# Kernel optimization log

Hardware: AMD Instinct MI355X
Metric: run time of the kernel (lower is better)

## Reference

```python
import jax, jax.numpy as jnp
import numpy as np

# ---- static config (matches init_kwargs) ----
B, N, DIM = 1, 2048, 1024
H, KVH, D = 16, 8, 64
GQ = H // KVH                 # grouped queries per kv head
WS = 64                       # sliding window size (causal, exact)
CBS, STRIDE = 32, 16          # compress block size / sliding stride
SEL_BLK, NSEL, NMEM = 32, 4, 1
NCB = N // STRIDE             # num compressed blocks (128)
NFB = N // SEL_BLK            # num fine blocks (64)
NCPF = SEL_BLK // STRIDE      # compressed blocks per fine block (2)
HID = CBS * D                 # compress MLP hidden (expand factor 1.0)
SCALE = D ** -0.5
THETA = 10000.0
NEG = -jnp.finfo(jnp.float32).max


def setup_inputs():
    key = jax.random.key(0)
    ks = jax.random.split(key, 16)
    s = 0.02
    r = lambda i, shape: jax.random.normal(ks[i], shape, jnp.float32) * s
    return {
        "inp": jax.random.normal(ks[0], (B, N, DIM), jnp.float32),
        "norm_g": jnp.ones((DIM,), jnp.float32),
        "Wqkv": r(1, (DIM, (H + 2 * KVH) * D)),
        "mem_kv": r(2, (2, KVH, NMEM, D)),
        "k_pos": r(3, (KVH, CBS, D)),
        "v_pos": r(4, (KVH, CBS, D)),
        "kW1": r(5, (CBS * D, HID)), "kb1": jnp.zeros((HID,), jnp.float32),
        "kW2": r(6, (HID, D)), "kb2": jnp.zeros((D,), jnp.float32),
        "vW1": r(7, (CBS * D, HID)), "vb1": jnp.zeros((HID,), jnp.float32),
        "vW2": r(8, (HID, D)), "vb2": jnp.zeros((D,), jnp.float32),
        "combW": r(9, (DIM, 3 * H)),
        "combB": jnp.tile(jnp.array([-2.0, -2.0, 2.0], jnp.float32), H),
        "Wout": r(10, (H * D, DIM)),
    }


def _rope(t):
    # lucidrains rotary-embedding-torch: interleaved adjacent-pair rotation
    inv_freq = 1.0 / (THETA ** (jnp.arange(0, D, 2, dtype=jnp.float32) / D))
    ang = jnp.arange(N, dtype=jnp.float32)[:, None] * inv_freq        # [N, D/2]
    cos = jnp.repeat(jnp.cos(ang), 2, axis=-1)                        # [N, D]
    sin = jnp.repeat(jnp.sin(ang), 2, axis=-1)
    t2 = t.reshape(*t.shape[:-1], D // 2, 2)
    rot = jnp.stack([-t2[..., 1], t2[..., 0]], axis=-1).reshape(t.shape)
    return t * cos + rot * sin


def _forward(inp, norm_g, Wqkv, mem_kv, k_pos, v_pos,
             kW1, kb1, kW2, kb2, vW1, vb1, vW2, vb2,
             combW, combB, Wout):
    # RMSNorm
    x = inp * jax.lax.rsqrt(jnp.mean(inp * inp, -1, keepdims=True)
                            + jnp.finfo(inp.dtype).eps) * norm_g
    qkv = x @ Wqkv
    q, k, v = jnp.split(qkv, [H * D, H * D + KVH * D], axis=-1)
    q = q.reshape(B, N, H, D).transpose(0, 2, 1, 3)      # b h n d
    k = k.reshape(B, N, KVH, D).transpose(0, 2, 1, 3)    # b kvh n d
    v = v.reshape(B, N, KVH, D).transpose(0, 2, 1, 3)

    # ---- compressed branch (overlapping windows, left zero pad) ----
    overlap = CBS - STRIDE
    kp = jnp.pad(k, ((0, 0), (0, 0), (overlap, 0), (0, 0)))
    vp = jnp.pad(v, ((0, 0), (0, 0), (overlap, 0), (0, 0)))
    widx = jnp.arange(NCB)[:, None] * STRIDE + jnp.arange(CBS)[None, :]  # [NCB, CBS]
    kw = kp[:, :, widx] + k_pos[None, :, None]   # b kvh w cbs d
    vw = vp[:, :, widx] + v_pos[None, :, None]

    def cmlp(t, W1, b1, W2, b2):
        t = t.reshape(B, KVH, NCB, CBS * D)
        return jax.nn.relu(t @ W1 + b1) @ W2 + b2       # b kvh w d

    ck = cmlp(kw, kW1, kb1, kW2, kb2)
    cv = cmlp(vw, vW1, vb1, vW2, vb2)
    ck = jnp.concatenate([jnp.broadcast_to(mem_kv[0], (B, KVH, NMEM, D)), ck], 2)
    cv = jnp.concatenate([jnp.broadcast_to(mem_kv[1], (B, KVH, NMEM, D)), cv], 2)

    qg = q.reshape(B, KVH, GQ, N, D)
    csim = jnp.einsum('bhgid,bhjd->bhgij', qg, ck) * SCALE   # no mask (cmask=None)
    cattn = jax.nn.softmax(csim, -1)
    cout = jnp.einsum('bhgij,bhjd->bhgid', cattn, cv).reshape(B, H, N, D)

    # rotary AFTER compressed attention (as in source)
    rq, rk = _rope(q), _rope(k)

    # ---- importance scores -> top-k fine block selection ----
    imp = csim[..., NMEM:].mean(2)                          # b kvh n NCB (share grouped q)
    imp = imp.reshape(B, KVH, N, NFB, NCPF).mean(-1)        # mean-pool to fine blocks
    q_blk = jnp.arange(N) // SEL_BLK
    diag = q_blk[:, None] == jnp.arange(NFB)[None, :]
    imp = jnp.where(diag[None, None], NEG, imp)             # mask own (diagonal) block
    imp = jax.nn.softmax(jnp.pad(imp, ((0, 0),) * 3 + ((1, 0),),
                                 constant_values=-1000.0), -1)[..., 1:]
    sel_val, sel_idx = jax.lax.top_k(imp, NSEL)             # b kvh n NSEL

    # ---- fine (block-selected) attention ----
    own = jnp.broadcast_to(q_blk[None, None, :, None], (B, KVH, N, 1))
    sel_idx = jnp.concatenate([sel_idx, own], -1)           # append own block
    fmask = jnp.repeat((sel_val > 1e-10)[..., None], SEL_BLK, -1)  # b kvh n NSEL blk
    causal_row = jnp.tril(jnp.ones((SEL_BLK, SEL_BLK), bool))[jnp.arange(N) % SEL_BLK]
    causal = jnp.broadcast_to(causal_row[None, None, :, None, :],
                              (B, KVH, N, 1, SEL_BLK))
    fmask = jnp.concatenate([fmask, causal], 3).reshape(B, KVH, N, (NSEL + 1) * SEL_BLK)

    fk_blocks = rk.reshape(B, KVH, NFB, SEL_BLK, D)
    fv_blocks = v.reshape(B, KVH, NFB, SEL_BLK, D)
    gather = jax.vmap(jax.vmap(lambda blocks, idx: blocks[idx]))  # over b, kvh
    fk = gather(fk_blocks, sel_idx).reshape(B, KVH, N, (NSEL + 1) * SEL_BLK, D)
    fv = gather(fv_blocks, sel_idx).reshape(B, KVH, N, (NSEL + 1) * SEL_BLK, D)

    rqg = rq.reshape(B, KVH, GQ, N, D)
    fsim = jnp.einsum('bhgid,bhijd->bhgij', rqg, fk) * SCALE
    fsim = jnp.where(fmask[:, :, None], fsim, NEG / 10)
    fattn = jax.nn.softmax(fsim, -1)
    fout = jnp.einsum('bhgij,bhijd->bhgid', fattn, fv).reshape(B, H, N, D)

    # ---- sliding window (causal, exact window size WS) ----
    NW = N // WS
    kp2 = jnp.pad(rk, ((0, 0), (0, 0), (WS, 0), (0, 0)))
    vp2 = jnp.pad(v, ((0, 0), (0, 0), (WS, 0), (0, 0)))
    kidx = jnp.arange(NW)[:, None] * WS + jnp.arange(2 * WS)[None, :]
    kwin = kp2[:, :, kidx]                                  # b kvh nw 2ws d
    vwin = vp2[:, :, kidx]
    qwin = rqg.reshape(B, KVH, GQ, NW, WS, D)
    ssim = jnp.einsum('bhgwid,bhwjd->bhgwij', qwin, kwin) * SCALE
    i = jnp.arange(WS)[:, None]
    j = jnp.arange(2 * WS)[None, :]
    diff = i - (j - WS)
    local_ok = (diff >= 0) & (diff < WS)                    # [WS, 2WS]
    keypos = jnp.arange(NW)[:, None, None] * WS + (jnp.arange(2 * WS) - WS)[None, None, :]
    smask = local_ok[None] & (keypos >= 0)                  # [NW, WS, 2WS]
    ssim = jnp.where(smask[None, None, None], ssim, NEG)
    sattn = jax.nn.softmax(ssim, -1)
    sout = jnp.einsum('bhgwij,bhwjd->bhgwid', sattn, vwin).reshape(B, H, N, D)

    # ---- learned strategy combination (compressed, fine, sliding) ----
    gates = jax.nn.sigmoid(x @ combW + combB).reshape(B, N, H, 3).transpose(0, 2, 1, 3)
    out = gates[..., 0:1] * cout + gates[..., 1:2] * fout + gates[..., 2:3] * sout
    out = out.transpose(0, 2, 1, 3).reshape(B, N, H * D) @ Wout
    return out


def reference(inp, norm_g, Wqkv, mem_kv, k_pos, v_pos,
              kW1, kb1, kW2, kb2, vW1, vb1, vW2, vb2,
              combW, combB, Wout):
    return _forward(inp, norm_g, Wqkv, mem_kv, k_pos, v_pos,
                    kW1, kb1, kW2, kb2, vW1, vb1, vW2, vb2,
                    combW, combB, Wout)
```

## Files before the change

### kernel.cpp

```cpp
#include <hip/hip_runtime.h>
#include <hip/hip_bf16.h>

#define NTOK 2048
#define DIM 1024
#define NH 16
#define KVH 8
#define GQ 2
#define HD 64
#define WS 64
#define CBS 32
#define STRIDE 16
#define SEL_BLK 32
#define NSEL 4
#define NMEM 1
#define NCB 128
#define NFB 64
#define HIDN 2048
#define SCALE 0.125f
#define NEGF (-3.4028234663852886e38f)
#define NEG10F (-3.4028234663852886e37f)

typedef __attribute__((ext_vector_type(8))) short bf16x8;
typedef __attribute__((ext_vector_type(4))) float f32x4;

__device__ __forceinline__ float bflo(unsigned u) { return __uint_as_float(u << 16); }
__device__ __forceinline__ float bfhi(unsigned u) { return __uint_as_float(u & 0xffff0000u); }
__device__ __forceinline__ void dot8(const float4& qa, const float4& qb, uint4 a, float& s) {
    s += qa.x * bflo(a.x) + qa.y * bfhi(a.x) + qa.z * bflo(a.y) + qa.w * bfhi(a.y) +
         qb.x * bflo(a.z) + qb.y * bfhi(a.z) + qb.z * bflo(a.w) + qb.w * bfhi(a.w);
}

__device__ __forceinline__ void gload_lds16(const void* g, void* l) {
    __builtin_amdgcn_global_load_lds((const __attribute__((address_space(1))) unsigned*)g,
                                     (__attribute__((address_space(3))) unsigned*)l, 16, 0, 0);
}

__device__ __forceinline__ void rms_body(const float* __restrict__ inp,
                                         const float* __restrict__ g,
                                         float* __restrict__ x,
                                         __hip_bfloat16* __restrict__ xb, int n) {
    const float* row = inp + (size_t)n * DIM;
    float ss = 0.f;
    for (int c = threadIdx.x; c < DIM; c += 256) { float v = row[c]; ss += v * v; }
    __shared__ float red[4];
    for (int o = 32; o; o >>= 1) ss += __shfl_down(ss, o, 64);
    if ((threadIdx.x & 63) == 0) red[threadIdx.x >> 6] = ss;
    __syncthreads();
    if (threadIdx.x == 0) red[0] = red[0] + red[1] + red[2] + red[3];
    __syncthreads();
    float rs = 1.0f / sqrtf(red[0] / (float)DIM + 1.1920928955078125e-07f);
    float* xr = x + (size_t)n * DIM;
    __hip_bfloat16* xbr = xb + (size_t)n * DIM;
    for (int c = threadIdx.x; c < DIM; c += 256) {
        float v = row[c] * rs * g[c];
        xr[c] = v;
        xbr[c] = __float2bfloat16(v);
    }
}

__device__ __forceinline__ void transpose_body(const float* __restrict__ B,
                                               __hip_bfloat16* __restrict__ Bt,
                                               int K, int N, int bx, int by) {
    __shared__ float tile[32][33];
    int n0 = bx * 32, k0 = by * 32;
    int x = threadIdx.x & 31, y = threadIdx.x >> 5;
    for (int i = 0; i < 4; i++) {
        int k = k0 + y + 8 * i, n = n0 + x;
        tile[y + 8 * i][x] = (k < K && n < N) ? B[(size_t)k * N + n] : 0.f;
    }
    __syncthreads();
    for (int i = 0; i < 4; i++) {
        int n = n0 + y + 8 * i, k = k0 + x;
        if (n < N && k < K) Bt[(size_t)n * K + k] = __float2bfloat16(tile[x][y + 8 * i]);
    }
}

__global__ __launch_bounds__(256) void pre_kernel(
    const float* inp, const float* norm_g, float* x, __hip_bfloat16* xb,
    const float* Wqkv, __hip_bfloat16* Wqkvt,
    const float* kW1, __hip_bfloat16* kW1t,
    const float* vW1, __hip_bfloat16* vW1t,
    const float* Wout, __hip_bfloat16* Woutt,
    const float* combW, __hip_bfloat16* combWt,
    const float* kW2, __hip_bfloat16* kW2t,
    const float* vW2, __hip_bfloat16* vW2t,
    const float* combB, float* gatesb,
    const float* kb2, float* ckraw,
    const float* vb2, float* cvraw) {
    int b = blockIdx.x;
    if (b < 2048) { rms_body(inp, norm_g, x, xb, b); return; }
    b -= 2048;
    if (b < 2048) { transpose_body(Wqkv, Wqkvt, 1024, 2048, b % 64, b / 64); return; }
    b -= 2048;
    if (b < 4096) { transpose_body(kW1, kW1t, 2048, 2048, b % 64, b / 64); return; }
    b -= 4096;
    if (b < 4096) { transpose_body(vW1, vW1t, 2048, 2048, b % 64, b / 64); return; }
    b -= 4096;
    if (b < 1024) { transpose_body(Wout, Woutt, 1024, 1024, b % 32, b / 32); return; }
    b -= 1024;
    if (b < 64) { transpose_body(combW, combWt, 1024, 48, b % 2, b / 2); return; }
    b -= 64;
    if (b < 128) { transpose_body(kW2, kW2t, 2048, 64, b % 2, b / 2); return; }
    b -= 128;
    if (b < 128) { transpose_body(vW2, vW2t, 2048, 64, b % 2, b / 2); return; }
    b -= 128;
    if (b < 384) {
        int idx = b * 256 + threadIdx.x;
        if (idx < 2048 * 48) gatesb[idx] = combB[idx % 48];
        return;
    }
    b -= 384;
    {
        int idx = b * 256 + threadIdx.x;
        int tot = 1024 * 64;
        if (idx < tot) ckraw[idx] = kb2[idx % 64];
        else if (idx < 2 * tot) { idx -= tot; cvraw[idx] = vb2[idx % 64]; }
        return;
    }
}
#define PRE_BLOCKS (2048 + 2048 + 4096 + 4096 + 1024 + 64 + 128 + 128 + 384 + 512)

template <int ACT, int OUTBF16>
__device__ __forceinline__ void mfma_gemm_body(const __hip_bfloat16* __restrict__ A,
                                               const __hip_bfloat16* __restrict__ Bt,
                                               const float* __restrict__ bias,
                                               void* __restrict__ Cp,
                                               int M, int N, int K, int bx, int by) {
    __shared__ __align__(16) short As[128 * 32];
    __shared__ __align__(16) short Bs[128 * 32];
    int tid = threadIdx.x;
    int lane = tid & 63, wave = tid >> 6;
    int wm = (wave >> 1) * 64, wn = (wave & 1) * 64;
    int m0 = by * 128, n0 = bx * 128;
    f32x4 acc[4][4];
    for (int r = 0; r < 4; r++)
        for (int c = 0; c < 4; c++)
            acc[r][c] = (f32x4){0.f, 0.f, 0.f, 0.f};

    int r0 = tid >> 2, kc0 = (tid & 3) * 8;
    int r1 = r0 + 64;

    for (int k0 = 0; k0 < K; k0 += 32) {
        __syncthreads();
        gload_lds16(A + (size_t)(m0 + r0) * K + k0 + kc0, &As[r0 * 32 + kc0]);
        gload_lds16(A + (size_t)(m0 + r1) * K + k0 + kc0, &As[r1 * 32 + kc0]);
        gload_lds16(Bt + (size_t)(n0 + r0) * K + k0 + kc0, &Bs[r0 * 32 + kc0]);
        gload_lds16(Bt + (size_t)(n0 + r1) * K + k0 + kc0, &Bs[r1 * 32 + kc0]);
        __syncthreads();
        bf16x8 af[4], bfr[4];
#pragma unroll
        for (int r = 0; r < 4; r++)
            af[r] = *(const bf16x8*)&As[(wm + r * 16 + (lane & 15)) * 32 + (lane >> 4) * 8];
#pragma unroll
        for (int c = 0; c < 4; c++)
            bfr[c] = *(const bf16x8*)&Bs[(wn + c * 16 + (lane & 15)) * 32 + (lane >> 4) * 8];
#pragma unroll
        for (int r = 0; r < 4; r++)
#pragma unroll
            for (int c = 0; c < 4; c++)
                acc[r][c] = __builtin_amdgcn_mfma_f32_16x16x32_bf16(af[r], bfr[c], acc[r][c], 0, 0, 0);
    }
    for (int r = 0; r < 4; r++) {
        int grow = m0 + wm + r * 16 + (lane >> 4) * 4;
        for (int c = 0; c < 4; c++) {
            int gcol = n0 + wn + c * 16 + (lane & 15);
            float bv = bias ? bias[gcol] : 0.f;
#pragma unroll
            for (int v = 0; v < 4; v++) {
                float val = acc[r][c][v] + bv;
                if (ACT == 1) val = fmaxf(val, 0.f);
                if (OUTBF16)
                    ((__hip_bfloat16*)Cp)[(size_t)(grow + v) * N + gcol] = __float2bfloat16(val);
                else
                    ((float*)Cp)[(size_t)(grow + v) * N + gcol] = val;
            }
        }
    }
}

template <int ACT, int OUTBF16>
__global__ __launch_bounds__(256) void mfma_gemm(const __hip_bfloat16* __restrict__ A,
                                                 const __hip_bfloat16* __restrict__ Bt,
                                                 const float* __restrict__ bias,
                                                 void* __restrict__ Cp,
                                                 int M, int N, int K) {
    mfma_gemm_body<ACT, OUTBF16>(A, Bt, bias, Cp, M, N, K, blockIdx.x, blockIdx.y);
}

__global__ __launch_bounds__(256) void mfma_gemm_pair(const __hip_bfloat16* A0,
                                                      const __hip_bfloat16* A1,
                                                      const __hip_bfloat16* Bt0,
                                                      const __hip_bfloat16* Bt1,
                                                      const float* bias0, const float* bias1,
                                                      __hip_bfloat16* C0, __hip_bfloat16* C1,
                                                      int M, int N, int K) {
    if (blockIdx.z == 0)
        mfma_gemm_body<1, 1>(A0, Bt0, bias0, C0, M, N, K, blockIdx.x, blockIdx.y);
    else
        mfma_gemm_body<1, 1>(A1, Bt1, bias1, C1, M, N, K, blockIdx.x, blockIdx.y);
}

__device__ __forceinline__ void skgemm_body(const __hip_bfloat16* __restrict__ A,
                                            const __hip_bfloat16* __restrict__ Bt,
                                            float* __restrict__ C,
                                            int M, int Nout, int K, int by, int bz, int nz) {
    __shared__ __align__(16) short As2[128 * 32];
    __shared__ __align__(16) short Bs2[64 * 32];
    int tid = threadIdx.x;
    int lane = tid & 63, wave = tid >> 6;
    int m0 = by * 128;
    int wm = wave * 32;
    int kchunk = K / nz;
    int kbase = bz * kchunk;
    f32x4 acc[2][4];
    for (int r = 0; r < 2; r++)
        for (int c = 0; c < 4; c++) acc[r][c] = (f32x4){0.f, 0.f, 0.f, 0.f};

    int ra = tid >> 2, kc = (tid & 3) * 8;
    int rb = ra < Nout ? ra : Nout - 1;
    for (int k0 = kbase; k0 < kbase + kchunk; k0 += 32) {
        __syncthreads();
        gload_lds16(A + (size_t)(m0 + ra) * K + k0 + kc, &As2[ra * 32 + kc]);
        gload_lds16(A + (size_t)(m0 + ra + 64) * K + k0 + kc, &As2[(ra + 64) * 32 + kc]);
        gload_lds16(Bt + (size_t)rb * K + k0 + kc, &Bs2[ra * 32 + kc]);
        __syncthreads();
        bf16x8 af[2], bfr[4];
#pragma unroll
        for (int r = 0; r < 2; r++)
            af[r] = *(const bf16x8*)&As2[(wm + r * 16 + (lane & 15)) * 32 + (lane >> 4) * 8];
#pragma unroll
        for (int c = 0; c < 4; c++)
            bfr[c] = *(const bf16x8*)&Bs2[(c * 16 + (lane & 15)) * 32 + (lane >> 4) * 8];
#pragma unroll
        for (int r = 0; r < 2; r++)
#pragma unroll
            for (int c = 0; c < 4; c++)
                acc[r][c] = __builtin_amdgcn_mfma_f32_16x16x32_bf16(af[r], bfr[c], acc[r][c], 0, 0, 0);
    }
    for (int r = 0; r < 2; r++) {
        int grow = m0 + wm + r * 16 + (lane >> 4) * 4;
        for (int c = 0; c < 4; c++) {
            int gcol = c * 16 + (lane & 15);
            if (gcol >= Nout) continue;
#pragma unroll
            for (int v = 0; v < 4; v++)
                atomicAdd(&C[(size_t)(grow + v) * Nout + gcol], acc[r][c][v]);
        }
    }
}

__global__ __launch_bounds__(256) void qkv_gates_kernel(const __hip_bfloat16* xb,
                                                        const __hip_bfloat16* Wqkvt,
                                                        float* qkv,
                                                        const __hip_bfloat16* combWt,
                                                        float* gatesb) {
    int b = blockIdx.x;
    if (b < 256) {
        mfma_gemm_body<0, 0>(xb, Wqkvt, nullptr, qkv, 2048, 2048, 1024, b & 15, b >> 4);
    } else {
        int s = b - 256;
        skgemm_body(xb, combWt, gatesb, 2048, 48, 1024, s & 15, s >> 4, 4);
    }
}

__global__ __launch_bounds__(256) void skgemm_pair(const __hip_bfloat16* A0,
                                                   const __hip_bfloat16* A1,
                                                   const __hip_bfloat16* Bt0,
                                                   const __hip_bfloat16* Bt1,
                                                   float* C0, float* C1,
                                                   int M, int Nout, int K) {
    if (blockIdx.x == 0)
        skgemm_body(A0, Bt0, C0, M, Nout, K, blockIdx.y, blockIdx.z, gridDim.z);
    else
        skgemm_body(A1, Bt1, C1, M, Nout, K, blockIdx.y, blockIdx.z, gridDim.z);
}

__global__ __launch_bounds__(256) void winrope_kernel(const float* __restrict__ qkv,
                                                      const float* __restrict__ k_pos,
                                                      const float* __restrict__ v_pos,
                                                      __hip_bfloat16* __restrict__ kwflat,
                                                      __hip_bfloat16* __restrict__ vwflat,
                                                      float* __restrict__ rq,
                                                      __hip_bfloat16* __restrict__ rk,
                                                      __hip_bfloat16* __restrict__ vt) {
    int b = blockIdx.x;
    int t = threadIdx.x;
    if (b < 4096) {
        size_t total = (size_t)(KVH * NCB) * HIDN;
        for (size_t e = (size_t)b * 256 + t; e < total; e += (size_t)4096 * 256) {
            int r = (int)(e >> 11);
            int c = (int)(e & 2047);
            int j = c >> 6, d = c & 63;
            int h = r >> 7, i = r & 127;
            int p = i * STRIDE + j - (CBS - STRIDE);
            float kb = k_pos[((size_t)h * CBS + j) * HD + d];
            float vb = v_pos[((size_t)h * CBS + j) * HD + d];
            float kv = 0.f, vv = 0.f;
            if (p >= 0) {
                kv = qkv[(size_t)p * 2048 + 1024 + h * HD + d];
                vv = qkv[(size_t)p * 2048 + 1536 + h * HD + d];
            }
            kwflat[e] = __float2bfloat16(kv + kb);
            vwflat[e] = __float2bfloat16(vv + vb);
        }
        return;
    }
    int n = b - 4096;
    for (int idx = t; idx < NH * 32; idx += 256) {
        int h = idx >> 5, f = idx & 31;
        float inv = exp2f((float)f * -0.41524101186092f);
        float ang = (float)n * inv;
        float cc = cosf(ang), ssn = sinf(ang);
        float a = qkv[(size_t)n * 2048 + h * HD + 2 * f];
        float bq = qkv[(size_t)n * 2048 + h * HD + 2 * f + 1];
        float* o = rq + ((size_t)h * NTOK + n) * HD + 2 * f;
        o[0] = a * cc - bq * ssn;
        o[1] = bq * cc + a * ssn;
    }
    for (int idx = t; idx < KVH * 32; idx += 256) {
        int h = idx >> 5, f = idx & 31;
        float inv = exp2f((float)f * -0.41524101186092f);
        float ang = (float)n * inv;
        float cc = cosf(ang), ssn = sinf(ang);
        float a = qkv[(size_t)n * 2048 + 1024 + h * HD + 2 * f];
        float bq = qkv[(size_t)n * 2048 + 1024 + h * HD + 2 * f + 1];
        __hip_bfloat16* o = rk + ((size_t)h * NTOK + n) * HD + 2 * f;
        o[0] = __float2bfloat16(a * cc - bq * ssn);
        o[1] = __float2bfloat16(bq * cc + a * ssn);
    }
    for (int idx = t; idx < KVH * HD; idx += 256) {
        int h = idx >> 6, d = idx & 63;
        vt[((size_t)h * NTOK + n) * HD + d] =
            __float2bfloat16(qkv[(size_t)n * 2048 + 1536 + h * HD + d]);
    }
}

__global__ __launch_bounds__(256) void cattn2_kernel(const float* __restrict__ qkv,
                                                     const float* __restrict__ ckraw,
                                                     const float* __restrict__ cvraw,
                                                     const float* __restrict__ memkv,
                                                     float* __restrict__ cout,
                                                     int* __restrict__ selidx,
                                                     int* __restrict__ selmask) {
    int h = blockIdx.x >> 6;
    int i0 = (blockIdx.x & 63) * 32;
    int t = threadIdx.x;
    __shared__ float qs[64][68];
    __shared__ float sc[64][132];
    __shared__ float scratch[32 * 68];
    __shared__ float memk[64], memv[64];

    for (int idx = t; idx < 4096; idx += 256) {
        int row = idx >> 6, d = idx & 63;
        int g = row >> 5, qi = row & 31;
        qs[row][d] = qkv[(size_t)(i0 + qi) * 2048 + (h * 2 + g) * 64 + d];
    }
    if (t < 64) { memk[t] = memkv[h * 64 + t]; memv[t] = memkv[(8 + h) * 64 + t]; }
    __syncthreads();
    if (t < 64) {
        float s = 0.f;
        for (int d = 0; d < 64; d++) s += qs[t][d] * memk[d];
        sc[t][0] = s * SCALE;
    }
    int rg = t >> 3, kg = t & 7;
    for (int c = 0; c < 4; c++) {
        __syncthreads();
        for (int idx = t; idx < 2048; idx += 256) {
            int jj = idx >> 6, d = idx & 63;
            scratch[jj * 68 + d] = ckraw[((size_t)h * 128 + c * 32 + jj) * 64 + d];
        }
        __syncthreads();
        float a0[4] = {}, a1[4] = {};
        for (int d = 0; d < 64; d += 4) {
            float4 q0 = *(const float4*)&qs[rg * 2][d];
            float4 q1 = *(const float4*)&qs[rg * 2 + 1][d];
#pragma unroll
            for (int kk = 0; kk < 4; kk++) {
                float4 kv = *(const float4*)&scratch[(kg + kk * 8) * 68 + d];
                a0[kk] += q0.x * kv.x + q0.y * kv.y + q0.z * kv.z + q0.w * kv.w;
                a1[kk] += q1.x * kv.x + q1.y * kv.y + q1.z * kv.z + q1.w * kv.w;
            }
        }
#pragma unroll
        for (int kk = 0; kk < 4; kk++) {
            sc[rg * 2][1 + c * 32 + kg + kk * 8] = a0[kk] * SCALE;
            sc[rg * 2 + 1][1 + c * 32 + kg + kk * 8] = a1[kk] * SCALE;
        }
    }
    __syncthreads();
    for (int idx = t; idx < 2048; idx += 256) {
        int qi = idx >> 6, fb = idx & 63;
        float v = 0.25f * (sc[qi][1 + 2 * fb] + sc[qi][2 + 2 * fb] +
                           sc[32 + qi][1 + 2 * fb] + sc[32 + qi][2 + 2 * fb]);
        if (fb == ((i0 + qi) >> 5)) v = NEGF;
        scratch[qi * 66 + fb] = v;
    }
    __syncthreads();
    if (t < 32) {
        float* row = &scratch[t * 66];
        float m = -1000.f;
        for (int j = 0; j < 64; j++) m = fmaxf(m, row[j]);
        float den = __expf(-1000.f - m);
        for (int j = 0; j < 64; j++) den += __expf(row[j] - m);
        float invd = 1.f / den;
        unsigned long long taken = 0ull;
        int mk = 0;
        size_t base = ((size_t)h * NTOK + i0 + t) * 5;
        for (int p = 0; p < NSEL; p++) {
            float bv = NEGF;
            int bi = 0;
            for (int j = 0; j < 64; j++) {
                if (!((taken >> j) & 1ull) && row[j] > bv) { bv = row[j]; bi = j; }
            }
            taken |= 1ull << bi;
            selidx[base + p] = bi;
            if (__expf(bv - m) * invd > 1e-10f) mk |= 1 << p;
        }
        selidx[base + 4] = (i0 + t) >> 5;
        selmask[h * NTOK + i0 + t] = mk;
    } else if (t >= 64 && t < 128) {
        int r = t - 64;
        float m = NEGF;
        for (int j = 0; j < 129; j++) m = fmaxf(m, sc[r][j]);
        float den = 0.f;
        for (int j = 0; j < 129; j++) { float e = __expf(sc[r][j] - m); sc[r][j] = e; den += e; }
        float inv = 1.f / den;
        for (int j = 0; j < 129; j++) sc[r][j] *= inv;
    }
    __syncthreads();
    int dg = t & 7;
    float o0[8], o1[8];
    {
        float p0 = sc[rg * 2][0], p1 = sc[rg * 2 + 1][0];
#pragma unroll
        for (int dd = 0; dd < 8; dd++) {
            float v = memv[dg + dd * 8];
            o0[dd] = p0 * v;
            o1[dd] = p1 * v;
        }
    }
    for (int c = 0; c < 4; c++) {
        __syncthreads();
        for (int idx = t; idx < 2048; idx += 256) {
            int jj = idx >> 6, d = idx & 63;
            scratch[jj * 68 + d] = cvraw[((size_t)h * 128 + c * 32 + jj) * 64 + d];
        }
        __syncthreads();
        for (int jj = 0; jj < 32; jj++) {
            float p0 = sc[rg * 2][1 + c * 32 + jj];
            float p1 = sc[rg * 2 + 1][1 + c * 32 + jj];
#pragma unroll
            for (int dd = 0; dd < 8; dd++) {
                float v = scratch[jj * 68 + dg + dd * 8];
                o0[dd] += p0 * v;
                o1[dd] += p1 * v;
            }
        }
    }
    {
        int row = rg * 2;
        int g = row >> 5, qi = row & 31;
        int g2 = (row + 1) >> 5, qi2 = (row + 1) & 31;
#pragma unroll
        for (int dd = 0; dd < 8; dd++) {
            cout[(((size_t)(h * 2 + g)) * NTOK + i0 + qi) * 64 + dd * 8 + dg] = o0[dd];
            cout[(((size_t)(h * 2 + g2)) * NTOK + i0 + qi2) * 64 + dd * 8 + dg] = o1[dd];
        }
    }
}

#define SWROWPAD 72
__global__ __launch_bounds__(256) void attn_fused2_kernel(const float* __restrict__ rq,
                                                          const __hip_bfloat16* __restrict__ rk,
                                                          const __hip_bfloat16* __restrict__ vt,
                                                          const int* __restrict__ selidx,
                                                          const int* __restrict__ selmask,
                                                          float* __restrict__ fout,
                                                          float* __restrict__ sout) {
    int tid = threadIdx.x;
    int ws = tid >> 6, lane = tid & 63;
    __shared__ __align__(16) char smem[2 * 128 * SWROWPAD * 2 + 4 * 128 * 4];
    __shared__ int sel[4][5];
    __shared__ int smk[4];

    int kq = lane >> 2, c = lane & 3;
    int kv8 = lane >> 3, c8 = lane & 7;

    if (blockIdx.x < 256) {
        int h = blockIdx.x >> 5;
        int q0 = (blockIdx.x & 31) * 64;
        short* ks = (short*)smem;
        short* vs = ks + 128 * SWROWPAD;
        float* ps = (float*)(vs + 128 * SWROWPAD);
        int basek = q0 - 63;
        for (int idx = tid; idx < 127 * 8; idx += 256) {
            int row = idx >> 3, ch = (idx & 7) * 8;
            int kpos = basek + row;
            uint4 kv = (uint4){0u, 0u, 0u, 0u}, vv = (uint4){0u, 0u, 0u, 0u};
            if (kpos >= 0) {
                kv = *(const uint4*)(rk + ((size_t)h * NTOK + kpos) * 64 + ch);
                vv = *(const uint4*)(vt + ((size_t)h * NTOK + kpos) * 64 + ch);
            }
            *(uint4*)&ks[row * SWROWPAD + ch] = kv;
            *(uint4*)&vs[row * SWROWPAD + ch] = vv;
        }
        __syncthreads();
        float* p0 = ps + ws * 128;
        float* p1 = p0 + 64;
#pragma unroll 1
        for (int tq = 0; tq < 16; tq++) {
            int i = q0 + ws * 16 + tq;
            int ibase = ws * 16 + tq;
            const float* q0p = rq + ((size_t)(h * 2 + 0) * NTOK + i) * 64 + c * 16;
            const float* q1p = rq + ((size_t)(h * 2 + 1) * NTOK + i) * 64 + c * 16;
            float4 qa[4], qb[4];
#pragma unroll
            for (int u = 0; u < 4; u++) {
                qa[u] = *(const float4*)(q0p + u * 4);
                qb[u] = *(const float4*)(q1p + u * 4);
            }
#pragma unroll
            for (int kt = 0; kt < 4; kt++) {
                int key = kt * 16 + kq;
                const short* kr = &ks[(ibase + key) * SWROWPAD + c * 16];
                float s0 = 0.f, s1 = 0.f;
                uint4 a = *(const uint4*)(kr);
                uint4 b = *(const uint4*)(kr + 8);
                dot8(qa[0], qa[1], a, s0); dot8(qa[2], qa[3], b, s0);
                dot8(qb[0], qb[1], a, s1); dot8(qb[2], qb[3], b, s1);
                s0 += __shfl_xor(s0, 1); s0 += __shfl_xor(s0, 2);
                s1 += __shfl_xor(s1, 1); s1 += __shfl_xor(s1, 2);
                int kpos = i - 63 + key;
                if (c == 0) {
                    p0[key] = (kpos >= 0) ? s0 * SCALE : NEG10F;
                    p1[key] = (kpos >= 0) ? s1 * SCALE : NEG10F;
                }
            }
            {
                float a0 = p0[lane], a1 = p1[lane];
                float m0 = a0, m1 = a1;
#pragma unroll
                for (int o = 1; o < 64; o <<= 1) {
                    m0 = fmaxf(m0, __shfl_xor(m0, o));
                    m1 = fmaxf(m1, __shfl_xor(m1, o));
                }
                float e0 = __expf(a0 - m0), e1 = __expf(a1 - m1);
                float d0 = e0, d1 = e1;
#pragma unroll
                for (int o = 1; o < 64; o <<= 1) {
                    d0 += __shfl_xor(d0, o);
                    d1 += __shfl_xor(d1, o);
                }
                p0[lane] = e0 / d0;
                p1[lane] = e1 / d1;
            }
            float o0[8] = {}, o1[8] = {};
#pragma unroll
            for (int pass = 0; pass < 8; pass++) {
                int j = pass * 8 + kv8;
                uint4 v = *(const uint4*)&vs[(ibase + j) * SWROWPAD + c8 * 8];
                float pa = p0[j], pb = p1[j];
                float e0 = bflo(v.x), e1 = bfhi(v.x), e2 = bflo(v.y), e3 = bfhi(v.y);
                float e4 = bflo(v.z), e5 = bfhi(v.z), e6 = bflo(v.w), e7 = bfhi(v.w);
                o0[0] = fmaf(pa, e0, o0[0]); o0[1] = fmaf(pa, e1, o0[1]);
                o0[2] = fmaf(pa, e2, o0[2]); o0[3] = fmaf(pa, e3, o0[3]);
                o0[4] = fmaf(pa, e4, o0[4]); o0[5] = fmaf(pa, e5, o0[5]);
                o0[6] = fmaf(pa, e6, o0[6]); o0[7] = fmaf(pa, e7, o0[7]);
                o1[0] = fmaf(pb, e0, o1[0]); o1[1] = fmaf(pb, e1, o1[1]);
                o1[2] = fmaf(pb, e2, o1[2]); o1[3] = fmaf(pb, e3, o1[3]);
                o1[4] = fmaf(pb, e4, o1[4]); o1[5] = fmaf(pb, e5, o1[5]);
                o1[6] = fmaf(pb, e6, o1[6]); o1[7] = fmaf(pb, e7, o1[7]);
            }
#pragma unroll
            for (int o = 8; o <= 32; o <<= 1)
#pragma unroll
                for (int d = 0; d < 8; d++) {
                    o0[d] += __shfl_xor(o0[d], o);
                    o1[d] += __shfl_xor(o1[d], o);
                }
            if (kv8 == 0) {
                float* s0p = sout + ((size_t)(h * 2 + 0) * NTOK + i) * 64 + c8 * 8;
                float* s1p = sout + ((size_t)(h * 2 + 1) * NTOK + i) * 64 + c8 * 8;
                *(float4*)(s0p) = (float4){o0[0], o0[1], o0[2], o0[3]};
                *(float4*)(s0p + 4) = (float4){o0[4], o0[5], o0[6], o0[7]};
                *(float4*)(s1p) = (float4){o1[0], o1[1], o1[2], o1[3]};
                *(float4*)(s1p + 4) = (float4){o1[4], o1[5], o1[6], o1[7]};
            }
        }
    } else {
        float* spbase = (float*)smem;
        float* p0 = spbase + ws * 320;
        float* p1 = p0 + 160;
        int wid = (blockIdx.x - 256) * 4 + ws;
        int h = wid >> 11, i = wid & 2047;
        if (lane < 5) sel[ws][lane] = selidx[((size_t)h * NTOK + i) * 5 + lane];
        if (lane == 5) smk[ws] = selmask[h * NTOK + i];

        const float* q0p = rq + ((size_t)(h * 2 + 0) * NTOK + i) * 64 + c * 16;
        const float* q1p = rq + ((size_t)(h * 2 + 1) * NTOK + i) * 64 + c * 16;
        float4 q0[4], q1[4];
#pragma unroll
        for (int u = 0; u < 4; u++) {
            q0[u] = *(const float4*)(q0p + u * 4);
            q1[u] = *(const float4*)(q1p + u * 4);
        }
        __syncthreads();
        int mk = smk[ws];
        int iq = i & 31;
#pragma unroll
        for (int kt = 0; kt < 10; kt++) {
            int slot = kt >> 1;
            int blk = sel[ws][slot];
            int key = kt * 16 + kq;
            int jj = key & 31;
            int kpos = blk * 32 + jj;
            bool valid = (slot < 4) ? (((mk >> slot) & 1) != 0) : (jj <= iq);
            const __hip_bfloat16* kr = rk + ((size_t)h * NTOK + kpos) * 64 + c * 16;
            float s0 = 0.f, s1 = 0.f;
            uint4 a = *(const uint4*)(kr);
            uint4 b = *(const uint4*)(kr + 8);
            dot8(q0[0], q0[1], a, s0); dot8(q0[2], q0[3], b, s0);
            dot8(q1[0], q1[1], a, s1); dot8(q1[2], q1[3], b, s1);
            s0 += __shfl_xor(s0, 1); s0 += __shfl_xor(s0, 2);
            s1 += __shfl_xor(s1, 1); s1 += __shfl_xor(s1, 2);
            if (c == 0) {
                p0[key] = valid ? s0 * SCALE : NEG10F;
                p1[key] = valid ? s1 * SCALE : NEG10F;
            }
        }
        __syncthreads();
        {
            float a0 = p0[lane], b0 = p0[lane + 64];
            float c0 = (lane < 32) ? p0[lane + 128] : NEG10F;
            float a1 = p1[lane], b1 = p1[lane + 64];
            float c1 = (lane < 32) ? p1[lane + 128] : NEG10F;
            float m0 = fmaxf(fmaxf(a0, b0), c0);
            float m1 = fmaxf(fmaxf(a1, b1), c1);
#pragma unroll
            for (int o = 1; o < 64; o <<= 1) {
                m0 = fmaxf(m0, __shfl_xor(m0, o));
                m1 = fmaxf(m1, __shfl_xor(m1, o));
            }
            float ea0 = __expf(a0 - m0), eb0 = __expf(b0 - m0), ec0 = (lane < 32) ? __expf(c0 - m0) : 0.f;
            float ea1 = __expf(a1 - m1), eb1 = __expf(b1 - m1), ec1 = (lane < 32) ? __expf(c1 - m1) : 0.f;
            float d0 = ea0 + eb0 + ec0;
            float d1 = ea1 + eb1 + ec1;
#pragma unroll
            for (int o = 1; o < 64; o <<= 1) {
                d0 += __shfl_xor(d0, o);
                d1 += __shfl_xor(d1, o);
            }
            float inv0 = 1.f / d0, inv1 = 1.f / d1;
            p0[lane] = ea0 * inv0; p0[lane + 64] = eb0 * inv0;
            p1[lane] = ea1 * inv1; p1[lane + 64] = eb1 * inv1;
            if (lane < 32) { p0[lane + 128] = ec0 * inv0; p1[lane + 128] = ec1 * inv1; }
        }
        __syncthreads();
        float o0[8] = {}, o1[8] = {};
#pragma unroll
        for (int slot = 0; slot < 5; slot++) {
            const __hip_bfloat16* vbase = vt + ((size_t)h * NTOK + sel[ws][slot] * 32) * 64;
#pragma unroll
            for (int pass = 0; pass < 4; pass++) {
                int j = pass * 8 + kv8;
                uint4 v = *(const uint4*)(vbase + j * 64 + c8 * 8);
                float pa = p0[slot * 32 + j], pb = p1[slot * 32 + j];
                float e0 = bflo(v.x), e1 = bfhi(v.x), e2 = bflo(v.y), e3 = bfhi(v.y);
                float e4 = bflo(v.z), e5 = bfhi(v.z), e6 = bflo(v.w), e7 = bfhi(v.w);
                o0[0] = fmaf(pa, e0, o0[0]); o0[1] = fmaf(pa, e1, o0[1]);
                o0[2] = fmaf(pa, e2, o0[2]); o0[3] = fmaf(pa, e3, o0[3]);
                o0[4] = fmaf(pa, e4, o0[4]); o0[5] = fmaf(pa, e5, o0[5]);
                o0[6] = fmaf(pa, e6, o0[6]); o0[7] = fmaf(pa, e7, o0[7]);
                o1[0] = fmaf(pb, e0, o1[0]); o1[1] = fmaf(pb, e1, o1[1]);
                o1[2] = fmaf(pb, e2, o1[2]); o1[3] = fmaf(pb, e3, o1[3]);
                o1[4] = fmaf(pb, e4, o1[4]); o1[5] = fmaf(pb, e5, o1[5]);
                o1[6] = fmaf(pb, e6, o1[6]); o1[7] = fmaf(pb, e7, o1[7]);
            }
        }
#pragma unroll
        for (int o = 8; o <= 32; o <<= 1)
#pragma unroll
            for (int d = 0; d < 8; d++) {
                o0[d] += __shfl_xor(o0[d], o);
                o1[d] += __shfl_xor(o1[d], o);
            }
        if (kv8 == 0) {
            float* f0 = fout + ((size_t)(h * 2 + 0) * NTOK + i) * 64 + c8 * 8;
            float* f1 = fout + ((size_t)(h * 2 + 1) * NTOK + i) * 64 + c8 * 8;
            *(float4*)(f0) = (float4){o0[0], o0[1], o0[2], o0[3]};
            *(float4*)(f0 + 4) = (float4){o0[4], o0[5], o0[6], o0[7]};
            *(float4*)(f1) = (float4){o1[0], o1[1], o1[2], o1[3]};
            *(float4*)(f1 + 4) = (float4){o1[4], o1[5], o1[6], o1[7]};
        }
    }
}

__global__ __launch_bounds__(256) void combine_kernel(const float* __restrict__ gateslin,
                                                      const float* __restrict__ cout,
                                                      const float* __restrict__ fout,
                                                      const float* __restrict__ sout,
                                                      __hip_bfloat16* __restrict__ att) {
    int n = blockIdx.x;
    for (int c = threadIdx.x; c < NH * HD; c += 256) {
        int hd = c >> 6, d = c & 63;
        float g0 = 1.f / (1.f + expf(-gateslin[(size_t)n * (NH * 3) + hd * 3 + 0]));
        float g1 = 1.f / (1.f + expf(-gateslin[(size_t)n * (NH * 3) + hd * 3 + 1]));
        float g2 = 1.f / (1.f + expf(-gateslin[(size_t)n * (NH * 3) + hd * 3 + 2]));
        size_t o = ((size_t)hd * NTOK + n) * HD + d;
        att[(size_t)n * (NH * HD) + c] =
            __float2bfloat16(g0 * cout[o] + g1 * fout[o] + g2 * sout[o]);
    }
}

extern "C" void kernel_launch(void* const* d_in, const int* in_sizes, int n_in,
                              void* d_out, int out_size, void* d_ws, size_t ws_size,
                              hipStream_t stream) {
    const float* inp    = (const float*)d_in[0];
    const float* norm_g = (const float*)d_in[1];
    const float* Wqkv   = (const float*)d_in[2];
    const float* mem_kv = (const float*)d_in[3];
    const float* k_pos  = (const float*)d_in[4];
    const float* v_pos  = (const float*)d_in[5];
    const float* kW1    = (const float*)d_in[6];
    const float* kb1    = (const float*)d_in[7];
    const float* kW2    = (const float*)d_in[8];
    const float* kb2    = (const float*)d_in[9];
    const float* vW1    = (const float*)d_in[10];
    const float* vb1    = (const float*)d_in[11];
    const float* vW2    = (const float*)d_in[12];
    const float* vb2    = (const float*)d_in[13];
    const float* combW  = (const float*)d_in[14];
    const float* combB  = (const float*)d_in[15];
    const float* Wout   = (const float*)d_in[16];
    float* out = (float*)d_out;

    char* base = (char*)d_ws;
    size_t off = 0;
    auto alloc = [&](size_t bytes) {
        void* p = base + off;
        off += (bytes + 255) & ~(size_t)255;
        return p;
    };
    float* x            = (float*)alloc((size_t)NTOK * DIM * 4);
    __hip_bfloat16* xb  = (__hip_bfloat16*)alloc((size_t)NTOK * DIM * 2);
    float* qkv          = (float*)alloc((size_t)NTOK * 2048 * 4);
    __hip_bfloat16* Wqkvt = (__hip_bfloat16*)alloc((size_t)2048 * 1024 * 2);
    __hip_bfloat16* kW1t  = (__hip_bfloat16*)alloc((size_t)2048 * 2048 * 2);
    __hip_bfloat16* vW1t  = (__hip_bfloat16*)alloc((size_t)2048 * 2048 * 2);
    __hip_bfloat16* Woutt = (__hip_bfloat16*)alloc((size_t)1024 * 1024 * 2);
    __hip_bfloat16* combWt = (__hip_bfloat16*)alloc((size_t)48 * 1024 * 2);
    __hip_bfloat16* kW2t  = (__hip_bfloat16*)alloc((size_t)64 * 2048 * 2);
    __hip_bfloat16* vW2t  = (__hip_bfloat16*)alloc((size_t)64 * 2048 * 2);
    __hip_bfloat16* kwflat = (__hip_bfloat16*)alloc((size_t)KVH * NCB * HIDN * 2);
    __hip_bfloat16* vwflat = (__hip_bfloat16*)alloc((size_t)KVH * NCB * HIDN * 2);
    __hip_bfloat16* hidkb = (__hip_bfloat16*)alloc((size_t)KVH * NCB * HIDN * 2);
    __hip_bfloat16* hidvb = (__hip_bfloat16*)alloc((size_t)KVH * NCB * HIDN * 2);
    float* ckraw        = (float*)alloc((size_t)KVH * NCB * HD * 4);
    float* cvraw        = (float*)alloc((size_t)KVH * NCB * HD * 4);
    float* rq           = (float*)alloc((size_t)NH * NTOK * HD * 4);
    __hip_bfloat16* rk  = (__hip_bfloat16*)alloc((size_t)KVH * NTOK * HD * 2);
    __hip_bfloat16* vt  = (__hip_bfloat16*)alloc((size_t)KVH * NTOK * HD * 2);
    float* coutb        = (float*)alloc((size_t)NH * NTOK * HD * 4);
    float* foutb        = (float*)alloc((size_t)NH * NTOK * HD * 4);
    float* soutb        = (float*)alloc((size_t)NH * NTOK * HD * 4);
    float* gatesb       = (float*)alloc((size_t)NTOK * NH * 3 * 4);
    __hip_bfloat16* attb = (__hip_bfloat16*)alloc((size_t)NTOK * DIM * 2);
    int* selidx         = (int*)alloc((size_t)KVH * NTOK * 5 * 4);
    int* selmask        = (int*)alloc((size_t)KVH * NTOK * 4);
    (void)ws_size; (void)in_sizes; (void)n_in; (void)out_size;

    pre_kernel<<<PRE_BLOCKS, 256, 0, stream>>>(inp, norm_g, x, xb,
                                               Wqkv, Wqkvt, kW1, kW1t, vW1, vW1t,
                                               Wout, Woutt, combW, combWt,
                                               kW2, kW2t, vW2, vW2t,
                                               combB, gatesb, kb2, ckraw, vb2, cvraw);
    qkv_gates_kernel<<<320, 256, 0, stream>>>(xb, Wqkvt, qkv, combWt, gatesb);
    winrope_kernel<<<4096 + 2048, 256, 0, stream>>>(qkv, k_pos, v_pos, kwflat, vwflat,
                                                    rq, rk, vt);
    mfma_gemm_pair<<<dim3(16, 8, 2), 256, 0, stream>>>(kwflat, vwflat, kW1t, vW1t,
                                                       kb1, vb1, hidkb, hidvb,
                                                       1024, 2048, 2048);
    skgemm_pair<<<dim3(2, 8, 8), 256, 0, stream>>>(hidkb, hidvb, kW2t, vW2t,
                                                   ckraw, cvraw, 1024, 64, 2048);
    cattn2_kernel<<<KVH * (NTOK / 32), 256, 0, stream>>>(qkv, ckraw, cvraw, mem_kv,
                                                         coutb, selidx, selmask);
    attn_fused2_kernel<<<256 + 4096, 256, 0, stream>>>(rq, rk, vt, selidx, selmask,
                                                       foutb, soutb);
    combine_kernel<<<NTOK, 256, 0, stream>>>(gatesb, coutb, foutb, soutb, attb);
    mfma_gemm<0, 0><<<dim3(8, 16), 256, 0, stream>>>(attb, Woutt, nullptr, out, 2048, 1024, 1024);
}
```

Baseline: 381.6 us.

## Merge sliding-window attention into per-query fine-attention warps

Before, the kernel had two branches: 256 blocks staged a K/V window in shared memory for sliding-window attention, and 4096 blocks did selected-block fine attention with one warp per query. Now each warp handles both fine and sliding attention for its own query, reusing the q registers and reading sliding-window K/V straight from global memory with the index clamped at the sequence start. The __syncthreads calls and the shared sel/mask arrays go away, since indices now live in registers. The cost is that overlapping window keys are re-read from global/L2 by each query rather than shared through LDS.

New measurement: 382.5 us. No clear change (+0.2%).

```diff
diff --git a/kernel.cpp b/kernel.cpp
--- a/kernel.cpp
+++ b/kernel.cpp
@@ -469,8 +469,7 @@
     }
 }
 
-#define SWROWPAD 72
-__global__ __launch_bounds__(256) void attn_fused2_kernel(const float* __restrict__ rq,
+__global__ __launch_bounds__(256) void attn_fused3_kernel(const float* __restrict__ rq,
                                                           const __hip_bfloat16* __restrict__ rk,
                                                           const __hip_bfloat16* __restrict__ vt,
                                                           const int* __restrict__ selidx,
@@ -479,87 +478,127 @@
                                                           float* __restrict__ sout) {
     int tid = threadIdx.x;
     int ws = tid >> 6, lane = tid & 63;
-    __shared__ __align__(16) char smem[2 * 128 * SWROWPAD * 2 + 4 * 128 * 4];
-    __shared__ int sel[4][5];
-    __shared__ int smk[4];
+    __shared__ float pbuf[4][448];
+    float* pf0 = pbuf[ws];
+    float* pf1 = pf0 + 160;
+    float* ps0 = pf0 + 320;
+    float* ps1 = pf0 + 384;
 
     int kq = lane >> 2, c = lane & 3;
     int kv8 = lane >> 3, c8 = lane & 7;
-
-    if (blockIdx.x < 256) {
-        int h = blockIdx.x >> 5;
-        int q0 = (blockIdx.x & 31) * 64;
-        short* ks = (short*)smem;
-        short* vs = ks + 128 * SWROWPAD;
-        float* ps = (float*)(vs + 128 * SWROWPAD);
-        int basek = q0 - 63;
-        for (int idx = tid; idx < 127 * 8; idx += 256) {
-            int row = idx >> 3, ch = (idx & 7) * 8;
-            int kpos = basek + row;
-            uint4 kv = (uint4){0u, 0u, 0u, 0u}, vv = (uint4){0u, 0u, 0u, 0u};
-            if (kpos >= 0) {
-                kv = *(const uint4*)(rk + ((size_t)h * NTOK + kpos) * 64 + ch);
-                vv = *(const uint4*)(vt + ((size_t)h * NTOK + kpos) * 64 + ch);
-            }
-            *(uint4*)&ks[row * SWROWPAD + ch] = kv;
-            *(uint4*)&vs[row * SWROWPAD + ch] = vv;
-        }
-        __syncthreads();
-        float* p0 = ps + ws * 128;
-        float* p1 = p0 + 64;
-#pragma unroll 1
-        for (int tq = 0; tq < 16; tq++) {
-            int i = q0 + ws * 16 + tq;
-            int ibase = ws * 16 + tq;
-            const float* q0p = rq + ((size_t)(h * 2 + 0) * NTOK + i) * 64 + c * 16;
-            const float* q1p = rq + ((size_t)(h * 2 + 1) * NTOK + i) * 64 + c * 16;
-            float4 qa[4], qb[4];
-#pragma unroll
-            for (int u = 0; u < 4; u++) {
-                qa[u] = *(const float4*)(q0p + u * 4);
-                qb[u] = *(const float4*)(q1p + u * 4);
-            }
-#pragma unroll
-            for (int kt = 0; kt < 4; kt++) {
-                int key = kt * 16 + kq;
-                const short* kr = &ks[(ibase + key) * SWROWPAD + c * 16];
-                float s0 = 0.f, s1 = 0.f;
-                uint4 a = *(const uint4*)(kr);
-                uint4 b = *(const uint4*)(kr + 8);
-                dot8(qa[0], qa[1], a, s0); dot8(qa[2], qa[3], b, s0);
-                dot8(qb[0], qb[1], a, s1); dot8(qb[2], qb[3], b, s1);
-                s0 += __shfl_xor(s0, 1); s0 += __shfl_xor(s0, 2);
-                s1 += __shfl_xor(s1, 1); s1 += __shfl_xor(s1, 2);
-                int kpos = i - 63 + key;
-                if (c == 0) {
-                    p0[key] = (kpos >= 0) ? s0 * SCALE : NEG10F;
-                    p1[key] = (kpos >= 0) ? s1 * SCALE : NEG10F;
-                }
-            }
-            {
-                float a0 = p0[lane], a1 = p1[lane];
-                float m0 = a0, m1 = a1;
-#pragma unroll
-                for (int o = 1; o < 64; o <<= 1) {
-                    m0 = fmaxf(m0, __shfl_xor(m0, o));
-                    m1 = fmaxf(m1, __shfl_xor(m1, o));
-                }
-                float e0 = __expf(a0 - m0), e1 = __expf(a1 - m1);
-                float d0 = e0, d1 = e1;
-#pragma unroll
-                for (int o = 1; o < 64; o <<= 1) {
-                    d0 += __shfl_xor(d0, o);
-                    d1 += __shfl_xor(d1, o);
-                }
-                p0[lane] = e0 / d0;
-                p1[lane] = e1 / d1;
-            }
-            float o0[8] = {}, o1[8] = {};
-#pragma unroll
-            for (int pass = 0; pass < 8; pass++) {
+    int wid = blockIdx.x * 4 + ws;
+    int h = wid >> 11, i = wid & 2047;
+
+    size_t sbase = ((size_t)h * NTOK + i) * 5;
+    int selr[5];
+#pragma unroll
+    for (int s = 0; s < 5; s++) selr[s] = selidx[sbase + s];
+    int mk = selmask[h * NTOK + i];
+
+    const float* q0p = rq + ((size_t)(h * 2 + 0) * NTOK + i) * 64 + c * 16;
+    const float* q1p = rq + ((size_t)(h * 2 + 1) * NTOK + i) * 64 + c * 16;
+    float4 q0[4], q1[4];
+#pragma unroll
+    for (int u = 0; u < 4; u++) {
+        q0[u] = *(const float4*)(q0p + u * 4);
+        q1[u] = *(const float4*)(q1p + u * 4);
+    }
+    int iq = i & 31;
+
+#pragma unroll
+    for (int kt = 0; kt < 10; kt++) {
+        int slot = kt >> 1;
+        int blk = selr[slot];
+        int key = kt * 16 + kq;
+        int jj = key & 31;
+        int kpos = blk * 32 + jj;
+        bool valid = (slot < 4) ? (((mk >> slot) & 1) != 0) : (jj <= iq);
+        const __hip_bfloat16* kr = rk + ((size_t)h * NTOK + kpos) * 64 + c * 16;
+        float s0 = 0.f, s1 = 0.f;
+        uint4 a = *(const uint4*)(kr);
+        uint4 b = *(const uint4*)(kr + 8);
+        dot8(q0[0], q0[1], a, s0); dot8(q0[2], q0[3], b, s0);
+        dot8(q1[0], q1[1], a, s1); dot8(q1[2], q1[3], b, s1);
+        s0 += __shfl_xor(s0, 1); s0 += __shfl_xor(s0, 2);
+        s1 += __shfl_xor(s1, 1); s1 += __shfl_xor(s1, 2);
+        if (c == 0) {
+            pf0[key] = valid ? s0 * SCALE : NEG10F;
+            pf1[key] = valid ? s1 * SCALE : NEG10F;
+        }
+    }
+#pragma unroll
+    for (int kt = 0; kt < 4; kt++) {
+        int koff = kt * 16 + kq;
+        int kpos = i - 63 + koff;
+        bool valid = kpos >= 0;
+        int kcl = valid ? kpos : 0;
+        const __hip_bfloat16* kr = rk + ((size_t)h * NTOK + kcl) * 64 + c * 16;
+        float s0 = 0.f, s1 = 0.f;
+        uint4 a = *(const uint4*)(kr);
+        uint4 b = *(const uint4*)(kr + 8);
+        dot8(q0[0], q0[1], a, s0); dot8(q0[2], q0[3], b, s0);
+        dot8(q1[0], q1[1], a, s1); dot8(q1[2], q1[3], b, s1);
+        s0 += __shfl_xor(s0, 1); s0 += __shfl_xor(s0, 2);
+        s1 += __shfl_xor(s1, 1); s1 += __shfl_xor(s1, 2);
+        if (c == 0) {
+            ps0[koff] = valid ? s0 * SCALE : NEG10F;
+            ps1[koff] = valid ? s1 * SCALE : NEG10F;
+        }
+    }
+    {
+        float a0 = pf0[lane], b0 = pf0[lane + 64];
+        float c0 = (lane < 32) ? pf0[lane + 128] : NEG10F;
+        float a1 = pf1[lane], b1 = pf1[lane + 64];
+        float c1 = (lane < 32) ? pf1[lane + 128] : NEG10F;
+        float m0 = fmaxf(fmaxf(a0, b0), c0);
+        float m1 = fmaxf(fmaxf(a1, b1), c1);
+#pragma unroll
+        for (int o = 1; o < 64; o <<= 1) {
+            m0 = fmaxf(m0, __shfl_xor(m0, o));
+            m1 = fmaxf(m1, __shfl_xor(m1, o));
+        }
+        float ea0 = __expf(a0 - m0), eb0 = __expf(b0 - m0), ec0 = (lane < 32) ? __expf(c0 - m0) : 0.f;
+        float ea1 = __expf(a1 - m1), eb1 = __expf(b1 - m1), ec1 = (lane < 32) ? __expf(c1 - m1) : 0.f;
+        float d0 = ea0 + eb0 + ec0;
+        float d1 = ea1 + eb1 + ec1;
+#pragma unroll
+        for (int o = 1; o < 64; o <<= 1) {
+            d0 += __shfl_xor(d0, o);
+            d1 += __shfl_xor(d1, o);
+        }
+        float inv0 = 1.f / d0, inv1 = 1.f / d1;
+        pf0[lane] = ea0 * inv0; pf0[lane + 64] = eb0 * inv0;
+        pf1[lane] = ea1 * inv1; pf1[lane + 64] = eb1 * inv1;
+        if (lane < 32) { pf0[lane + 128] = ec0 * inv0; pf1[lane + 128] = ec1 * inv1; }
+    }
+    {
+        float a0 = ps0[lane], a1 = ps1[lane];
+        float m0 = a0, m1 = a1;
+#pragma unroll
+        for (int o = 1; o < 64; o <<= 1) {
+            m0 = fmaxf(m0, __shfl_xor(m0, o));
+            m1 = fmaxf(m1, __shfl_xor(m1, o));
+        }
+        float e0 = __expf(a0 - m0), e1 = __expf(a1 - m1);
+        float d0 = e0, d1 = e1;
+#pragma unroll
+        for (int o = 1; o < 64; o <<= 1) {
+            d0 += __shfl_xor(d0, o);
+            d1 += __shfl_xor(d1, o);
+        }
+        ps0[lane] = e0 / d0;
+        ps1[lane] = e1 / d1;
+    }
+    {
+        float o0[8] = {}, o1[8] = {};
+#pragma unroll
+        for (int slot = 0; slot < 5; slot++) {
+            const __hip_bfloat16* vbase = vt + ((size_t)h * NTOK + selr[slot] * 32) * 64;
+#pragma unroll
+            for (int pass = 0; pass < 4; pass++) {
                 int j = pass * 8 + kv8;
-                uint4 v = *(const uint4*)&vs[(ibase + j) * SWROWPAD + c8 * 8];
-                float pa = p0[j], pb = p1[j];
+                uint4 v = *(const uint4*)(vbase + j * 64 + c8 * 8);
+                float pa = pf0[slot * 32 + j], pb = pf1[slot * 32 + j];
                 float e0 = bflo(v.x), e1 = bfhi(v.x), e2 = bflo(v.y), e3 = bfhi(v.y);
                 float e4 = bflo(v.z), e5 = bfhi(v.z), e6 = bflo(v.w), e7 = bfhi(v.w);
                 o0[0] = fmaf(pa, e0, o0[0]); o0[1] = fmaf(pa, e1, o0[1]);
@@ -571,111 +610,6 @@
                 o1[4] = fmaf(pb, e4, o1[4]); o1[5] = fmaf(pb, e5, o1[5]);
                 o1[6] = fmaf(pb, e6, o1[6]); o1[7] = fmaf(pb, e7, o1[7]);
             }
-#pragma unroll
-            for (int o = 8; o <= 32; o <<= 1)
-#pragma unroll
-                for (int d = 0; d < 8; d++) {
-                    o0[d] += __shfl_xor(o0[d], o);
-                    o1[d] += __shfl_xor(o1[d], o);
-                }
-            if (kv8 == 0) {
-                float* s0p = sout + ((size_t)(h * 2 + 0) * NTOK + i) * 64 + c8 * 8;
-                float* s1p = sout + ((size_t)(h * 2 + 1) * NTOK + i) * 64 + c8 * 8;
-                *(float4*)(s0p) = (float4){o0[0], o0[1], o0[2], o0[3]};
-                *(float4*)(s0p + 4) = (float4){o0[4], o0[5], o0[6], o0[7]};
-                *(float4*)(s1p) = (float4){o1[0], o1[1], o1[2], o1[3]};
-                *(float4*)(s1p + 4) = (float4){o1[4], o1[5], o1[6], o1[7]};
-            }
-        }
-    } else {
-        float* spbase = (float*)smem;
-        float* p0 = spbase + ws * 320;
-        float* p1 = p0 + 160;
-        int wid = (blockIdx.x - 256) * 4 + ws;
-        int h = wid >> 11, i = wid & 2047;
-        if (lane < 5) sel[ws][lane] = selidx[((size_t)h * NTOK + i) * 5 + lane];
-        if (lane == 5) smk[ws] = selmask[h * NTOK + i];
-
-        const float* q0p = rq + ((size_t)(h * 2 + 0) * NTOK + i) * 64 + c * 16;
-        const float* q1p = rq + ((size_t)(h * 2 + 1) * NTOK + i) * 64 + c * 16;
-        float4 q0[4], q1[4];
-#pragma unroll
-        for (int u = 0; u < 4; u++) {
-            q0[u] = *(const float4*)(q0p + u * 4);
-            q1[u] = *(const float4*)(q1p + u * 4);
-        }
-        __syncthreads();
-        int mk = smk[ws];
-        int iq = i & 31;
-#pragma unroll
-        for (int kt = 0; kt < 10; kt++) {
-            int slot = kt >> 1;
-            int blk = sel[ws][slot];
-            int key = kt * 16 + kq;
-            int jj = key & 31;
-            int kpos = blk * 32 + jj;
-            bool valid = (slot < 4) ? (((mk >> slot) & 1) != 0) : (jj <= iq);
-            const __hip_bfloat16* kr = rk + ((size_t)h * NTOK + kpos) * 64 + c * 16;
-            float s0 = 0.f, s1 = 0.f;
-            uint4 a = *(const uint4*)(kr);
-            uint4 b = *(const uint4*)(kr + 8);
-            dot8(q0[0], q0[1], a, s0); dot8(q0[2], q0[3], b, s0);
-            dot8(q1[0], q1[1], a, s1); dot8(q1[2], q1[3], b, s1);
-            s0 += __shfl_xor(s0, 1); s0 += __shfl_xor(s0, 2);
-            s1 += __shfl_xor(s1, 1); s1 += __shfl_xor(s1, 2);
-            if (c == 0) {
-                p0[key] = valid ? s0 * SCALE : NEG10F;
-                p1[key] = valid ? s1 * SCALE : NEG10F;
-            }
-        }
-        __syncthreads();
-        {
-            float a0 = p0[lane], b0 = p0[lane + 64];
-            float c0 = (lane < 32) ? p0[lane + 128] : NEG10F;
-            float a1 = p1[lane], b1 = p1[lane + 64];
-            float c1 = (lane < 32) ? p1[lane + 128] : NEG10F;
-            float m0 = fmaxf(fmaxf(a0, b0), c0);
-            float m1 = fmaxf(fmaxf(a1, b1), c1);
-#pragma unroll
-            for (int o = 1; o < 64; o <<= 1) {
-                m0 = fmaxf(m0, __shfl_xor(m0, o));
-                m1 = fmaxf(m1, __shfl_xor(m1, o));
-            }
-            float ea0 = __expf(a0 - m0), eb0 = __expf(b0 - m0), ec0 = (lane < 32) ? __expf(c0 - m0) : 0.f;
-            float ea1 = __expf(a1 - m1), eb1 = __expf(b1 - m1), ec1 = (lane < 32) ? __expf(c1 - m1) : 0.f;
-            float d0 = ea0 + eb0 + ec0;
-            float d1 = ea1 + eb1 + ec1;
-#pragma unroll
-            for (int o = 1; o < 64; o <<= 1) {
-                d0 += __shfl_xor(d0, o);
-                d1 += __shfl_xor(d1, o);
-            }
-            float inv0 = 1.f / d0, inv1 = 1.f / d1;
-            p0[lane] = ea0 * inv0; p0[lane + 64] = eb0 * inv0;
-            p1[lane] = ea1 * inv1; p1[lane + 64] = eb1 * inv1;
-            if (lane < 32) { p0[lane + 128] = ec0 * inv0; p1[lane + 128] = ec1 * inv1; }
-        }
-        __syncthreads();
-        float o0[8] = {}, o1[8] = {};
-#pragma unroll
-        for (int slot = 0; slot < 5; slot++) {
-            const __hip_bfloat16* vbase = vt + ((size_t)h * NTOK + sel[ws][slot] * 32) * 64;
-#pragma unroll
-            for (int pass = 0; pass < 4; pass++) {
-                int j = pass * 8 + kv8;
-                uint4 v = *(const uint4*)(vbase + j * 64 + c8 * 8);
-                float pa = p0[slot * 32 + j], pb = p1[slot * 32 + j];
-                float e0 = bflo(v.x), e1 = bfhi(v.x), e2 = bflo(v.y), e3 = bfhi(v.y);
-                float e4 = bflo(v.z), e5 = bfhi(v.z), e6 = bflo(v.w), e7 = bfhi(v.w);
-                o0[0] = fmaf(pa, e0, o0[0]); o0[1] = fmaf(pa, e1, o0[1]);
-                o0[2] = fmaf(pa, e2, o0[2]); o0[3] = fmaf(pa, e3, o0[3]);
-                o0[4] = fmaf(pa, e4, o0[4]); o0[5] = fmaf(pa, e5, o0[5]);
-                o0[6] = fmaf(pa, e6, o0[6]); o0[7] = fmaf(pa, e7, o0[7]);
-                o1[0] = fmaf(pb, e0, o1[0]); o1[1] = fmaf(pb, e1, o1[1]);
-                o1[2] = fmaf(pb, e2, o1[2]); o1[3] = fmaf(pb, e3, o1[3]);
-                o1[4] = fmaf(pb, e4, o1[4]); o1[5] = fmaf(pb, e5, o1[5]);
-                o1[6] = fmaf(pb, e6, o1[6]); o1[7] = fmaf(pb, e7, o1[7]);
-            }
         }
 #pragma unroll
         for (int o = 8; o <= 32; o <<= 1)
@@ -691,6 +625,42 @@
             *(float4*)(f0 + 4) = (float4){o0[4], o0[5], o0[6], o0[7]};
             *(float4*)(f1) = (float4){o1[0], o1[1], o1[2], o1[3]};
             *(float4*)(f1 + 4) = (float4){o1[4], o1[5], o1[6], o1[7]};
+        }
+    }
+    {
+        float o0[8] = {}, o1[8] = {};
+#pragma unroll
+        for (int pass = 0; pass < 8; pass++) {
+            int j = pass * 8 + kv8;
+            int kpos = i - 63 + j;
+            int kcl = kpos >= 0 ? kpos : 0;
+            uint4 v = *(const uint4*)(vt + ((size_t)h * NTOK + kcl) * 64 + c8 * 8);
+            float pa = ps0[j], pb = ps1[j];
+            float e0 = bflo(v.x), e1 = bfhi(v.x), e2 = bflo(v.y), e3 = bfhi(v.y);
+            float e4 = bflo(v.z), e5 = bfhi(v.z), e6 = bflo(v.w), e7 = bfhi(v.w);
+            o0[0] = fmaf(pa, e0, o0[0]); o0[1] = fmaf(pa, e1, o0[1]);
+            o0[2] = fmaf(pa, e2, o0[2]); o0[3] = fmaf(pa, e3, o0[3]);
+            o0[4] = fmaf(pa, e4, o0[4]); o0[5] = fmaf(pa, e5, o0[5]);
+            o0[6] = fmaf(pa, e6, o0[6]); o0[7] = fmaf(pa, e7, o0[7]);
+            o1[0] = fmaf(pb, e0, o1[0]); o1[1] = fmaf(pb, e1, o1[1]);
+            o1[2] = fmaf(pb, e2, o1[2]); o1[3] = fmaf(pb, e3, o1[3]);
+            o1[4] = fmaf(pb, e4, o1[4]); o1[5] = fmaf(pb, e5, o1[5]);
+            o1[6] = fmaf(pb, e6, o1[6]); o1[7] = fmaf(pb, e7, o1[7]);
+        }
+#pragma unroll
+        for (int o = 8; o <= 32; o <<= 1)
+#pragma unroll
+            for (int d = 0; d < 8; d++) {
+                o0[d] += __shfl_xor(o0[d], o);
+                o1[d] += __shfl_xor(o1[d], o);
+            }
+        if (kv8 == 0) {
+            float* s0p = sout + ((size_t)(h * 2 + 0) * NTOK + i) * 64 + c8 * 8;
+            float* s1p = sout + ((size_t)(h * 2 + 1) * NTOK + i) * 64 + c8 * 8;
+            *(float4*)(s0p) = (float4){o0[0], o0[1], o0[2], o0[3]};
+            *(float4*)(s0p + 4) = (float4){o0[4], o0[5], o0[6], o0[7]};
+            *(float4*)(s1p) = (float4){o1[0], o1[1], o1[2], o1[3]};
+            *(float4*)(s1p + 4) = (float4){o1[4], o1[5], o1[6], o1[7]};
         }
     }
 }
@@ -784,8 +754,8 @@
                                                    ckraw, cvraw, 1024, 64, 2048);
     cattn2_kernel<<<KVH * (NTOK / 32), 256, 0, stream>>>(qkv, ckraw, cvraw, mem_kv,
                                                          coutb, selidx, selmask);
-    attn_fused2_kernel<<<256 + 4096, 256, 0, stream>>>(rq, rk, vt, selidx, selmask,
-                                                       foutb, soutb);
+    attn_fused3_kernel<<<4096, 256, 0, stream>>>(rq, rk, vt, selidx, selmask,
+                                                 foutb, soutb);
     combine_kernel<<<NTOK, 256, 0, stream>>>(gatesb, coutb, foutb, soutb, attb);
     mfma_gemm<0, 0><<<dim3(8, 16), 256, 0, stream>>>(attb, Woutt, nullptr, out, 2048, 1024, 1024);
 }
```
